# Kernel tuning notes

Measured on AMD Instinct MI355X. Metric: run time of the kernel, lower is better.

## Reference

```python
import jax, jax.numpy as jnp
import numpy as np

N = 25000      # nodes per type
E = 300000     # weight-edge rows
K = 16         # neighbors
F = 64         # in_feat
A = 64         # atten_dim
DW = 64        # weight_dim
CB = 8         # num_bit_conv
CV = 8         # num_vector_conv
OUT = 64       # out_feat
IN_K = CB * F + CV * (3 + 2 + 1)


def setup_inputs() -> dict:
    key = jax.random.key(0)
    ks = jax.random.split(key, 40)
    s = 0.05
    d = {}
    d['eu'] = jax.random.normal(ks[0], (N, F), jnp.float32)
    d['ei'] = jax.random.normal(ks[1], (N, F), jnp.float32)
    d['et'] = jax.random.normal(ks[2], (N, F), jnp.float32)
    d['ew'] = jax.random.normal(ks[3], (E, DW), jnp.float32)
    names = ['u_iw_j', 'u_tw_j', 'i_uw_j', 'i_tw_j', 't_uw_j', 't_iw_j']
    for i, nm in enumerate(names):
        d[nm] = jax.random.randint(ks[4 + i], (N, K), 0, N, jnp.int64 if jax.config.jax_enable_x64 else jnp.int32)
        d[nm.replace('_j', '_w')] = jax.random.randint(ks[10 + i], (N, K), 0, E, jnp.int64 if jax.config.jax_enable_x64 else jnp.int32)
    # per-type Attention1 params: user, item, tag
    for i, t in enumerate(['user', 'item', 'tag']):
        b = 16 + 4 * i
        d[f'W1_{t}'] = jax.random.normal(ks[b], (F + DW, A), jnp.float32) * s
        d[f'W2_{t}'] = jax.random.normal(ks[b + 1], (F, A), jnp.float32) * s
        d[f'b_{t}'] = jax.random.normal(ks[b + 2], (1, A), jnp.float32) * s
        d[f'v_{t}'] = jax.random.normal(ks[b + 3], (1, A), jnp.float32) * s
    d['U'] = jax.random.normal(ks[28], (F, A), jnp.float32) * s
    d['q'] = jax.random.normal(ks[29], (1, A), jnp.float32) * s
    d['p'] = jax.random.normal(ks[30], (1, A), jnp.float32) * s
    d['W_bit'] = jax.random.normal(ks[31], (CB, 3), jnp.float32) * s       # Conv2d(1,CB,(3,1))
    d['W_vec1'] = jax.random.normal(ks[32], (CV, 1, F), jnp.float32) * s   # Conv2d(1,CV,(1,F))
    d['W_vec2'] = jax.random.normal(ks[33], (CV, 2, F), jnp.float32) * s
    d['W_vec3'] = jax.random.normal(ks[34], (CV, 3, F), jnp.float32) * s
    d['Wf'] = jax.random.normal(ks[35], (IN_K, OUT), jnp.float32) * s
    d['bf'] = jax.random.normal(ks[36], (1, OUT), jnp.float32) * s
    return d


def _atten1(ev, ej, ew, v_j, v_w, W1, W2, b, v):
    ejp = jnp.concatenate([jnp.zeros((1, ej.shape[1]), ej.dtype), ej], axis=0)
    ewp = jnp.concatenate([jnp.zeros((1, ew.shape[1]), ew.dtype), ew], axis=0)
    eNj = ejp[v_j]                                  # [N,K,F]
    eNw = ewp[v_w]                                  # [N,K,DW]
    eNv = jnp.broadcast_to(ev[:, None, :], (ev.shape[0], v_j.shape[1], ev.shape[1]))
    eN_vw = jnp.concatenate([eNv, eNw], axis=-1)    # [N,K,F+DW]
    av = jnp.einsum('nkd,da->nka', eN_vw, W1) + jnp.einsum('nkf,fa->nka', eNj, W2) + b
    x = jax.nn.relu(av) @ v.T                       # [N,K,1]
    a = jax.nn.softmax(x, axis=1)
    return jnp.sum(a * eNj, axis=1)                 # [N,F]


def _atten2(u, i, t, U, q, p):
    uit = jnp.stack([u, i, t], axis=1)              # [N,3,F]
    x = jnp.einsum('nsf,fa->nsa', uit, U) + q
    x = jax.nn.relu(x) @ p.T                        # [N,3,1]
    b = jax.nn.softmax(x, axis=1)
    return b * uit                                  # [N,3,F]


def _conv(eN, W_bit, W_vec1, W_vec2, W_vec3):
    # eN: [N,3,F]
    bit = jax.nn.relu(jnp.einsum('njf,cj->ncf', eN, W_bit))       # [N,CB,F]
    bit = bit.reshape(bit.shape[0], -1)
    vec = []
    for j, W in ((1, W_vec1), (2, W_vec2), (3, W_vec3)):
        win = jnp.stack([eN[:, s:s + j, :] for s in range(3 - j + 1)], axis=1)  # [N,4-j,j,F]
        y = jax.nn.relu(jnp.einsum('nsjf,cjf->ncs', win, W))       # [N,CV,4-j]
        vec.append(y.reshape(y.shape[0], -1))
    return jnp.concatenate([bit] + vec, axis=1)                    # [N,IN_K]


def _forward(eu, ei, et, ew, params, idx):
    (W1u, W2u, bu, vu, W1i, W2i, bi, vi, W1t, W2t, bt, vt,
     U, q, p, W_bit, W_vec1, W_vec2, W_vec3, Wf, bf) = params
    (u_iw_j, u_iw_w, u_tw_j, u_tw_w, i_uw_j, i_uw_w,
     i_tw_j, i_tw_w, t_uw_j, t_uw_w, t_iw_j, t_iw_w) = idx
    eu_iN = _atten1(eu, ei, ew, u_iw_j, u_iw_w, W1i, W2i, bi, vi)
    eu_tN = _atten1(eu, et, ew, u_tw_j, u_tw_w, W1t, W2t, bt, vt)
    ei_uN = _atten1(ei, eu, ew, i_uw_j, i_uw_w, W1u, W2u, bu, vu)
    ei_tN = _atten1(ei, et, ew, i_tw_j, i_tw_w, W1t, W2t, bt, vt)
    et_uN = _atten1(et, eu, ew, t_uw_j, t_uw_w, W1u, W2u, bu, vu)
    et_iN = _atten1(et, ei, ew, t_iw_j, t_iw_w, W1i, W2i, bi, vi)
    euN = _atten2(eu, eu_iN, eu_tN, U, q, p)
    eiN = _atten2(ei_uN, ei, ei_tN, U, q, p)
    etN = _atten2(et_uN, et_iN, et, U, q, p)
    out = []
    for eN in (euN, eiN, etN):
        c = _conv(eN, W_bit, W_vec1, W_vec2, W_vec3)
        out.append(jax.nn.relu(c @ Wf + bf))
    return tuple(out)


def reference(eu, ei, et, ew,
              u_iw_j, u_iw_w, u_tw_j, u_tw_w, i_uw_j, i_uw_w, i_tw_j, i_tw_w,
              t_uw_j, t_uw_w, t_iw_j, t_iw_w,
              W1_user, W2_user, b_user, v_user,
              W1_item, W2_item, b_item, v_item,
              W1_tag, W2_tag, b_tag, v_tag,
              U, q, p, W_bit, W_vec1, W_vec2, W_vec3, Wf, bf):
    params = (W1_user, W2_user, b_user, v_user, W1_item, W2_item, b_item, v_item,
              W1_tag, W2_tag, b_tag, v_tag, U, q, p, W_bit, W_vec1, W_vec2, W_vec3, Wf, bf)
    idx = (u_iw_j, u_iw_w, u_tw_j, u_tw_w, i_uw_j, i_uw_w,
           i_tw_j, i_tw_w, t_uw_j, t_uw_w, t_iw_j, t_iw_w)
    return _forward(eu, ei, et, ew, params, idx)
```

## Files before the change

kernel.cpp:

```cpp
#include <hip/hip_runtime.h>
#include <math.h>

#define NN 25000
#define EE 300000
#define NT 1563
#define NT64 391
#define ET64 4688

typedef __attribute__((ext_vector_type(8))) short bf16x8;
typedef __attribute__((ext_vector_type(4))) float f32x4;
typedef __attribute__((ext_vector_type(2))) float f32x2;

__device__ __forceinline__ unsigned short f2bf(float f) {
    union { float f; unsigned u; } a; a.f = f;
    unsigned r = (a.u + 0x7fffu + ((a.u >> 16) & 1u)) >> 16;
    return (unsigned short)r;
}
__device__ __forceinline__ unsigned pack2(float lo, float hi) {
    return (unsigned)f2bf(lo) | ((unsigned)f2bf(hi) << 16);
}
__device__ __forceinline__ float bflo(unsigned p) {
    union { unsigned u; float f; } a; a.u = p << 16; return a.f;
}
__device__ __forceinline__ float bfhi(unsigned p) {
    union { unsigned u; float f; } a; a.u = p & 0xffff0000u; return a.f;
}
__device__ __forceinline__ unsigned packfp8x4(float a, float b, float c, float d) {
    int v = __builtin_amdgcn_cvt_pk_fp8_f32(a, b, 0, 0);
    v = __builtin_amdgcn_cvt_pk_fp8_f32(c, d, v, 1);
    return (unsigned)v;
}

__global__ __launch_bounds__(256) void head_kernel(
    const float* __restrict__ ew,
    const float* __restrict__ eu, const float* __restrict__ ei, const float* __restrict__ et,
    const float* __restrict__ W1u, const float* __restrict__ W1i, const float* __restrict__ W1t,
    const float* __restrict__ W2u, const float* __restrict__ W2i, const float* __restrict__ W2t,
    const float* __restrict__ bu, const float* __restrict__ bi, const float* __restrict__ bt,
    unsigned char* __restrict__ gw8, unsigned* __restrict__ preB,
    unsigned char* __restrict__ JG)
{
    __shared__ __align__(16) unsigned short stA[64 * 72];
    __shared__ __align__(16) float cS[64 * 68];
    const int t = threadIdx.x;
    const int lane = t & 63, wv = t >> 6;
    const int l15 = lane & 15, quad = lane >> 4;
    const int cw = wv * 16 + l15;
    const int bx = blockIdx.x;

    if (bx < ET64) {
        if (bx == 0 && t < 48) {
            int w = t >> 4;
            ((unsigned*)(gw8 + (size_t)w * (EE + 1) * 64))[t & 15] = 0u;
        }
        const float* Ws[3] = { W1u + 4096, W1i + 4096, W1t + 4096 };
        bf16x8 bf[3][2];
        #pragma unroll
        for (int w = 0; w < 3; ++w)
            #pragma unroll
            for (int ks = 0; ks < 2; ++ks)
                #pragma unroll
                for (int j = 0; j < 8; ++j)
                    bf[w][ks][j] = (short)f2bf(Ws[w][(ks * 32 + quad * 8 + j) * 64 + cw]);

        const int rowBase = bx * 64;
        #pragma unroll
        for (int i = 0; i < 4; ++i) {
            int idx = t + i * 256;
            int row = idx >> 4, cg = idx & 15;
            int gr = rowBase + row;
            float4 v4 = (gr < EE) ? *(const float4*)(ew + (size_t)gr * 64 + cg * 4)
                                  : make_float4(0.f, 0.f, 0.f, 0.f);
            uint2 pk = { pack2(v4.x, v4.y), pack2(v4.z, v4.w) };
            *(uint2*)&stA[row * 72 + cg * 4] = pk;
        }
        __syncthreads();
        bf16x8 af[4][2];
        #pragma unroll
        for (int m = 0; m < 4; ++m)
            #pragma unroll
            for (int ks = 0; ks < 2; ++ks)
                af[m][ks] = *(const bf16x8*)&stA[(m * 16 + l15) * 72 + ks * 32 + quad * 8];

        #pragma unroll
        for (int w = 0; w < 3; ++w) {
            if (w) __syncthreads();
            f32x4 acc[4];
            #pragma unroll
            for (int m = 0; m < 4; ++m) {
                acc[m].x = 0; acc[m].y = 0; acc[m].z = 0; acc[m].w = 0;
                #pragma unroll
                for (int ks = 0; ks < 2; ++ks)
                    acc[m] = __builtin_amdgcn_mfma_f32_16x16x32_bf16(af[m][ks], bf[w][ks], acc[m], 0, 0, 0);
                #pragma unroll
                for (int r = 0; r < 4; ++r)
                    cS[(m * 16 + quad * 4 + r) * 68 + cw] = acc[m][r];
            }
            __syncthreads();
            unsigned char* outg = gw8 + (size_t)w * (EE + 1) * 64 + 64;
            #pragma unroll
            for (int i = 0; i < 2; ++i) {
                int task = t + i * 256;
                int row = task >> 3, seg = task & 7;
                int gr = rowBase + row;
                if (gr < EE) {
                    float4 a = *(const float4*)&cS[row * 68 + seg * 8];
                    float4 b = *(const float4*)&cS[row * 68 + seg * 8 + 4];
                    uint2 pk = { packfp8x4(a.x, a.y, a.z, a.w),
                                 packfp8x4(b.x, b.y, b.z, b.w) };
                    *(uint2*)(outg + (size_t)gr * 64 + seg * 8) = pk;
                }
            }
        }
    } else {
        const int yy = bx - ET64;
        const int y = yy / NT64;
        const int rowBase = (yy - y * NT64) * 64;
        if (rowBase == 0 && t < 48)
            ((unsigned*)(JG + (size_t)y * (NN + 1) * 192))[t] = 0u;
        const float* X; const float* Wa; const float* Wb; const float* W2;
        const float* ba; const float* bb; int oa, ob;
        switch (y) {
            case 0:  X = eu; Wa = W1i; ba = bi; oa = 0; Wb = W1t; bb = bt; ob = 1; W2 = W2u; break;
            case 1:  X = ei; Wa = W1u; ba = bu; oa = 2; Wb = W1t; bb = bt; ob = 3; W2 = W2i; break;
            default: X = et; Wa = W1u; ba = bu; oa = 4; Wb = W1i; bb = bi; ob = 5; W2 = W2t; break;
        }
        const float* Ws[3] = { Wa, Wb, W2 };
        const float bias_cw[3] = { ba[cw], bb[cw], 0.f };
        bf16x8 bf[3][2];
        #pragma unroll
        for (int w = 0; w < 3; ++w)
            #pragma unroll
            for (int ks = 0; ks < 2; ++ks)
                #pragma unroll
                for (int j = 0; j < 8; ++j)
                    bf[w][ks][j] = (short)f2bf(Ws[w][(ks * 32 + quad * 8 + j) * 64 + cw]);

        #pragma unroll
        for (int i = 0; i < 4; ++i) {
            int idx = t + i * 256;
            int row = idx >> 4, cg = idx & 15;
            int gr = rowBase + row;
            float4 v4 = (gr < NN) ? *(const float4*)(X + (size_t)gr * 64 + cg * 4)
                                  : make_float4(0.f, 0.f, 0.f, 0.f);
            uint2 pk = { pack2(v4.x, v4.y), pack2(v4.z, v4.w) };
            *(uint2*)&stA[row * 72 + cg * 4] = pk;
        }
        __syncthreads();
        bf16x8 af[4][2];
        #pragma unroll
        for (int m = 0; m < 4; ++m)
            #pragma unroll
            for (int ks = 0; ks < 2; ++ks)
                af[m][ks] = *(const bf16x8*)&stA[(m * 16 + l15) * 72 + ks * 32 + quad * 8];

        #pragma unroll
        for (int w = 0; w < 3; ++w) {
            if (w) __syncthreads();
            f32x4 acc[4];
            #pragma unroll
            for (int m = 0; m < 4; ++m) {
                acc[m].x = 0; acc[m].y = 0; acc[m].z = 0; acc[m].w = 0;
                #pragma unroll
                for (int ks = 0; ks < 2; ++ks)
                    acc[m] = __builtin_amdgcn_mfma_f32_16x16x32_bf16(af[m][ks], bf[w][ks], acc[m], 0, 0, 0);
                #pragma unroll
                for (int r = 0; r < 4; ++r)
                    cS[(m * 16 + quad * 4 + r) * 68 + cw] = acc[m][r] + bias_cw[w];
            }
            __syncthreads();
            #pragma unroll
            for (int i = 0; i < 2; ++i) {
                int task = t + i * 256;
                int row = task >> 3, seg = task & 7;
                int gr = rowBase + row;
                if (gr >= NN) continue;
                float4 a = *(const float4*)&cS[row * 68 + seg * 8];
                float4 b = *(const float4*)&cS[row * 68 + seg * 8 + 4];
                if (w < 2) {
                    int oi = (w == 0) ? oa : ob;
                    uint4 pk = { pack2(a.x, a.y), pack2(a.z, a.w),
                                 pack2(b.x, b.y), pack2(b.z, b.w) };
                    *(uint4*)(preB + ((size_t)oi * NN + gr) * 32 + seg * 4) = pk;
                } else {
                    unsigned char* dst = JG + ((size_t)y * (NN + 1) + gr + 1) * 192;
                    uint2 gj = { packfp8x4(a.x, a.y, a.z, a.w),
                                 packfp8x4(b.x, b.y, b.z, b.w) };
                    *(uint2*)(dst + seg * 8) = gj;
                    uint4 ej = *(const uint4*)&stA[row * 72 + seg * 8];
                    *(uint4*)(dst + 64 + seg * 16) = ej;
                }
            }
        }
    }
}

__global__ __launch_bounds__(256) void atten1_kernel(
    const unsigned* __restrict__ preB, const unsigned char* __restrict__ gw8,
    const unsigned char* __restrict__ JG,
    const float* __restrict__ vu, const float* __restrict__ vi, const float* __restrict__ vt,
    const int* __restrict__ u_iw_j, const int* __restrict__ u_iw_w,
    const int* __restrict__ u_tw_j, const int* __restrict__ u_tw_w,
    const int* __restrict__ i_uw_j, const int* __restrict__ i_uw_w,
    const int* __restrict__ i_tw_j, const int* __restrict__ i_tw_w,
    const int* __restrict__ t_uw_j, const int* __restrict__ t_uw_w,
    const int* __restrict__ t_iw_j, const int* __restrict__ t_iw_w,
    unsigned* __restrict__ aoB)
{
    const int y = blockIdx.y;
    const int* Vj; const int* Vw; const float* v; int g;
    switch (y) {
        case 0:  Vj = u_iw_j; Vw = u_iw_w; v = vi; g = 1; break;
        case 1:  Vj = u_tw_j; Vw = u_tw_w; v = vt; g = 2; break;
        case 2:  Vj = i_uw_j; Vw = i_uw_w; v = vu; g = 0; break;
        case 3:  Vj = i_tw_j; Vw = i_tw_w; v = vt; g = 2; break;
        case 4:  Vj = t_uw_j; Vw = t_uw_w; v = vu; g = 0; break;
        default: Vj = t_iw_j; Vw = t_iw_w; v = vi; g = 1; break;
    }
    const unsigned* pre = preB + (size_t)y * NN * 32;
    const unsigned char* gw = gw8 + (size_t)g * (EE + 1) * 64;
    const unsigned char* jg = JG + (size_t)g * (NN + 1) * 192;
    unsigned*            out = aoB + (size_t)y * NN * 32;

    const int lane = threadIdx.x & 63;
    const int n = blockIdx.x * 4 + (threadIdx.x >> 6);
    const int q = lane >> 4, r = lane & 15;

    const uint2 prep = *(const uint2*)(pre + (size_t)n * 32 + 2 * r);
    const float pf0 = bflo(prep.x), pf1 = bfhi(prep.x);
    const float pf2 = bflo(prep.y), pf3 = bfhi(prep.y);
    const float4 v4 = *(const float4*)(v + r * 4);

    const int4 wi = *(const int4*)(Vw + n * 16 + q * 4);
    const int4 ji = *(const int4*)(Vj + n * 16 + q * 4);
    const int wid[4] = { wi.x, wi.y, wi.z, wi.w };
    const int jid[4] = { ji.x, ji.y, ji.z, ji.w };

    unsigned gwv[4], gjv[4]; uint2 ejv[4];
    #pragma unroll
    for (int i = 0; i < 4; ++i)
        gwv[i] = *(const unsigned*)(gw + (size_t)wid[i] * 64 + r * 4);
    #pragma unroll
    for (int i = 0; i < 4; ++i) {
        const unsigned char* row = jg + (size_t)jid[i] * 192;
        gjv[i] = *(const unsigned*)(row + r * 4);
        ejv[i] = *(const uint2*)(row + 64 + r * 8);
    }

    float xk[4];
    #pragma unroll
    for (int i = 0; i < 4; ++i) {
        f32x2 g01 = __builtin_amdgcn_cvt_pk_f32_fp8((int)gwv[i], false);
        f32x2 g23 = __builtin_amdgcn_cvt_pk_f32_fp8((int)gwv[i], true);
        f32x2 j01 = __builtin_amdgcn_cvt_pk_f32_fp8((int)gjv[i], false);
        f32x2 j23 = __builtin_amdgcn_cvt_pk_f32_fp8((int)gjv[i], true);
        float x =          fmaxf(pf0 + g01.x + j01.x, 0.f) * v4.x;
        x = fmaf(fmaxf(pf1 + g01.y + j01.y, 0.f), v4.y, x);
        x = fmaf(fmaxf(pf2 + g23.x + j23.x, 0.f), v4.z, x);
        x = fmaf(fmaxf(pf3 + g23.y + j23.y, 0.f), v4.w, x);
        x += __shfl_xor(x, 1, 64);
        x += __shfl_xor(x, 2, 64);
        x += __shfl_xor(x, 4, 64);
        x += __shfl_xor(x, 8, 64);
        xk[i] = x;
    }
    float m = fmaxf(fmaxf(xk[0], xk[1]), fmaxf(xk[2], xk[3]));
    m = fmaxf(m, __shfl_xor(m, 16, 64));
    m = fmaxf(m, __shfl_xor(m, 32, 64));
    float e0 = __expf(xk[0] - m), e1 = __expf(xk[1] - m);
    float e2 = __expf(xk[2] - m), e3 = __expf(xk[3] - m);
    float s = (e0 + e1) + (e2 + e3);
    s += __shfl_xor(s, 16, 64);
    s += __shfl_xor(s, 32, 64);
    const float inv = 1.f / s;

    float a0 = 0.f, a1 = 0.f, a2 = 0.f, a3 = 0.f;
    const float wgt[4] = { e0 * inv, e1 * inv, e2 * inv, e3 * inv };
    #pragma unroll
    for (int i = 0; i < 4; ++i) {
        a0 = fmaf(wgt[i], bflo(ejv[i].x), a0);
        a1 = fmaf(wgt[i], bfhi(ejv[i].x), a1);
        a2 = fmaf(wgt[i], bflo(ejv[i].y), a2);
        a3 = fmaf(wgt[i], bfhi(ejv[i].y), a3);
    }
    a0 += __shfl_xor(a0, 16, 64); a0 += __shfl_xor(a0, 32, 64);
    a1 += __shfl_xor(a1, 16, 64); a1 += __shfl_xor(a1, 32, 64);
    a2 += __shfl_xor(a2, 16, 64); a2 += __shfl_xor(a2, 32, 64);
    a3 += __shfl_xor(a3, 16, 64); a3 += __shfl_xor(a3, 32, 64);
    if (q == 0) {
        uint2 pk = { pack2(a0, a1), pack2(a2, a3) };
        *(uint2*)(out + (size_t)n * 32 + 2 * r) = pk;
    }
}

__global__ __launch_bounds__(256, 3) void tail_kernel(
    const float* __restrict__ eu, const float* __restrict__ ei, const float* __restrict__ et,
    const unsigned* __restrict__ aoB,
    const float* __restrict__ U, const float* __restrict__ q, const float* __restrict__ p,
    const float* __restrict__ Wbit, const float* __restrict__ Wv1,
    const float* __restrict__ Wv2, const float* __restrict__ Wv3,
    const float* __restrict__ Wf, const float* __restrict__ bfv,
    float* __restrict__ out)
{
    __shared__ __align__(16) unsigned short uitA[48 * 72];
    __shared__ __align__(16) unsigned short eNA[48 * 72];
    __shared__ __align__(16) unsigned short wcf[6 * 64 * 8];
    __shared__ __align__(16) unsigned short c_sh[16 * 584];
    __shared__ float G_sh[48 * 52];
    __shared__ float xpart[4 * 48];
    __shared__ float bcoef[16 * 4];

    const int t = threadIdx.x;
    const int lane = t & 63;
    const int wv = t >> 6;
    const int l15 = lane & 15;
    const int quad = lane >> 4;
    const int type = blockIdx.y;
    const float* xf = (type == 0) ? eu : (type == 1) ? ei : et;
    const int cw = wv * 16 + l15;
    const float qv = q[cw], pv = p[cw], bfb = bfv[cw];

    float wb[8][3];
    #pragma unroll
    for (int c = 0; c < 8; ++c)
        #pragma unroll
        for (int s = 0; s < 3; ++s) wb[c][s] = Wbit[c * 3 + s];

    bf16x8 ufrag[2];
    #pragma unroll
    for (int ks = 0; ks < 2; ++ks)
        #pragma unroll
        for (int j = 0; j < 8; ++j) {
            int f = ks * 32 + quad * 8 + j;
            ufrag[ks][j] = (short)f2bf(U[f * 64 + cw]);
        }
    bf16x8 wff[18];
    #pragma unroll
    for (int ks = 0; ks < 18; ++ks)
        #pragma unroll
        for (int j = 0; j < 8; ++j) {
            int k = ks * 32 + quad * 8 + j;
            float w = (k < 560) ? Wf[(size_t)k * 64 + cw] : 0.f;
            wff[ks][j] = (short)f2bf(w);
        }
    for (int slot = t; slot < 384; slot += 256) {
        int fi = slot >> 6, l = slot & 63;
        int nt_ = fi >> 1, ks = fi & 1;
        int r = nt_ * 16 + (l & 15);
        unsigned short vals[8];
        #pragma unroll
        for (int j = 0; j < 8; ++j) {
            int f = ks * 32 + (l >> 4) * 8 + j;
            float wv_;
            if (r < 8)       wv_ = Wv1[r * 64 + f];
            else if (r < 24) { int u = r - 8;  wv_ = Wv2[(u >> 1) * 128 + (u & 1) * 64 + f]; }
            else             { int u = r - 24; wv_ = Wv3[(u / 3) * 192 + (u % 3) * 64 + f]; }
            vals[j] = f2bf(wv_);
        }
        uint4 pk = { (unsigned)vals[0] | ((unsigned)vals[1] << 16),
                     (unsigned)vals[2] | ((unsigned)vals[3] << 16),
                     (unsigned)vals[4] | ((unsigned)vals[5] << 16),
                     (unsigned)vals[6] | ((unsigned)vals[7] << 16) };
        *(uint4*)&wcf[slot * 8] = pk;
    }

    for (int tile = blockIdx.x; tile < NT; tile += gridDim.x) {
        const int nodeBase = tile * 16;
        __syncthreads();
        #pragma unroll
        for (int i = 0; i < 3; ++i) {
            int idx = t + i * 256;
            int row = idx >> 4, cg = idx & 15;
            int nl = row / 3, s = row - nl * 3;
            int n = nodeBase + nl;
            uint2 pk;
            if (s == type) {
                float4 v4 = (n < NN) ? *(const float4*)(xf + (size_t)n * 64 + cg * 4)
                                     : make_float4(0.f, 0.f, 0.f, 0.f);
                pk.x = pack2(v4.x, v4.y); pk.y = pack2(v4.z, v4.w);
            } else {
                int aoidx = (type == 0) ? (s - 1)
                          : (type == 1) ? ((s == 0) ? 2 : 3)
                                        : ((s == 0) ? 4 : 5);
                pk = (n < NN) ? *(const uint2*)(aoB + ((size_t)aoidx * NN + n) * 32 + cg * 2)
                              : make_uint2(0u, 0u);
            }
            *(uint2*)&uitA[row * 72 + cg * 4] = pk;
        }
        __syncthreads();
        {
            f32x4 av[3];
            #pragma unroll
            for (int mt = 0; mt < 3; ++mt) { av[mt].x = 0; av[mt].y = 0; av[mt].z = 0; av[mt].w = 0; }
            #pragma unroll
            for (int mt = 0; mt < 3; ++mt)
                #pragma unroll
                for (int ks = 0; ks < 2; ++ks) {
                    bf16x8 a = *(const bf16x8*)&uitA[(mt * 16 + l15) * 72 + ks * 32 + quad * 8];
                    av[mt] = __builtin_amdgcn_mfma_f32_16x16x32_bf16(a, ufrag[ks], av[mt], 0, 0, 0);
                }
            #pragma unroll
            for (int mt = 0; mt < 3; ++mt)
                #pragma unroll
                for (int r = 0; r < 4; ++r) {
                    float val = fmaxf(av[mt][r] + qv, 0.f) * pv;
                    val += __shfl_xor(val, 1, 64); val += __shfl_xor(val, 2, 64);
                    val += __shfl_xor(val, 4, 64); val += __shfl_xor(val, 8, 64);
                    if (l15 == 0) xpart[wv * 48 + mt * 16 + quad * 4 + r] = val;
                }
        }
        __syncthreads();
        if (t < 16) {
            float xv[3];
            #pragma unroll
            for (int s = 0; s < 3; ++s)
                xv[s] = xpart[t * 3 + s] + xpart[48 + t * 3 + s]
                      + xpart[96 + t * 3 + s] + xpart[144 + t * 3 + s];
            float mm = fmaxf(xv[0], fmaxf(xv[1], xv[2]));
            float e0 = __expf(xv[0] - mm), e1 = __expf(xv[1] - mm), e2 = __expf(xv[2] - mm);
            float inv = 1.f / (e0 + e1 + e2);
            bcoef[t * 4 + 0] = e0 * inv; bcoef[t * 4 + 1] = e1 * inv; bcoef[t * 4 + 2] = e2 * inv;
        }
        __syncthreads();
        #pragma unroll
        for (int i = 0; i < 2; ++i) {
            int task = t + i * 256;
            int nl = task >> 5, fp = task & 31;
            float b0 = bcoef[nl * 4], b1 = bcoef[nl * 4 + 1], b2 = bcoef[nl * 4 + 2];
            unsigned u0 = *(const unsigned*)&uitA[(nl * 3 + 0) * 72 + fp * 2];
            unsigned u1 = *(const unsigned*)&uitA[(nl * 3 + 1) * 72 + fp * 2];
            unsigned u2 = *(const unsigned*)&uitA[(nl * 3 + 2) * 72 + fp * 2];
            float e0l = b0 * bflo(u0), e0h = b0 * bfhi(u0);
            float e1l = b1 * bflo(u1), e1h = b1 * bfhi(u1);
            float e2l = b2 * bflo(u2), e2h = b2 * bfhi(u2);
            *(unsigned*)&eNA[(nl * 3 + 0) * 72 + fp * 2] = pack2(e0l, e0h);
            *(unsigned*)&eNA[(nl * 3 + 1) * 72 + fp * 2] = pack2(e1l, e1h);
            *(unsigned*)&eNA[(nl * 3 + 2) * 72 + fp * 2] = pack2(e2l, e2h);
            #pragma unroll
            for (int c = 0; c < 8; ++c) {
                float lo = fmaxf(wb[c][0] * e0l + wb[c][1] * e1l + wb[c][2] * e2l, 0.f);
                float hi = fmaxf(wb[c][0] * e0h + wb[c][1] * e1h + wb[c][2] * e2h, 0.f);
                *(unsigned*)&c_sh[nl * 584 + c * 64 + fp * 2] = pack2(lo, hi);
            }
        }
        __syncthreads();
        #pragma unroll
        for (int pi = 0; pi < 3; ++pi) {
            int pr = wv + pi * 4;
            if (pr < 9) {
                int mm = pr / 3, nn_ = pr - mm * 3;
                f32x4 g; g.x = 0; g.y = 0; g.z = 0; g.w = 0;
                #pragma unroll
                for (int ks = 0; ks < 2; ++ks) {
                    bf16x8 a = *(const bf16x8*)&eNA[(mm * 16 + l15) * 72 + ks * 32 + quad * 8];
                    bf16x8 b = *(const bf16x8*)&wcf[((nn_ * 2 + ks) * 64 + lane) * 8];
                    g = __builtin_amdgcn_mfma_f32_16x16x32_bf16(a, b, g, 0, 0, 0);
                }
                #pragma unroll
                for (int r = 0; r < 4; ++r)
                    G_sh[(mm * 16 + quad * 4 + r) * 52 + nn_ * 16 + l15] = g[r];
            }
        }
        __syncthreads();
        #pragma unroll
        for (int i = 0; i < 4; ++i) {
            int task = t + i * 256;
            int vvv = task >> 4, nl = task & 15;
            unsigned short res = 0;
            if (vvv < 24) {
                int c = vvv / 3, s = vvv - c * 3;
                res = f2bf(fmaxf(G_sh[(nl * 3 + s) * 52 + c], 0.f));
            } else if (vvv < 40) {
                int u = vvv - 24, c = u >> 1, s = u & 1;
                float val = G_sh[(nl * 3 + s) * 52 + 8 + 2 * c]
                          + G_sh[(nl * 3 + s + 1) * 52 + 8 + 2 * c + 1];
                res = f2bf(fmaxf(val, 0.f));
            } else if (vvv < 48) {
                int c = vvv - 40;
                float val = G_sh[(nl * 3 + 0) * 52 + 24 + 3 * c]
                          + G_sh[(nl * 3 + 1) * 52 + 24 + 3 * c + 1]
                          + G_sh[(nl * 3 + 2) * 52 + 24 + 3 * c + 2];
                res = f2bf(fmaxf(val, 0.f));
            }
            c_sh[nl * 584 + 512 + vvv] = res;
        }
        __syncthreads();
        {
            f32x4 acc; acc.x = 0; acc.y = 0; acc.z = 0; acc.w = 0;
            const unsigned short* ap = &c_sh[l15 * 584 + quad * 8];
            #pragma unroll
            for (int ks = 0; ks < 18; ++ks) {
                bf16x8 a = *(const bf16x8*)(ap + ks * 32);
                acc = __builtin_amdgcn_mfma_f32_16x16x32_bf16(a, wff[ks], acc, 0, 0, 0);
            }
            float* outT = out + (size_t)type * NN * 64;
            #pragma unroll
            for (int r = 0; r < 4; ++r) {
                int node = nodeBase + quad * 4 + r;
                if (node < NN) outT[(size_t)node * 64 + cw] = fmaxf(acc[r] + bfb, 0.f);
            }
        }
    }
}

extern "C" void kernel_launch(void* const* d_in, const int* in_sizes, int n_in,
                              void* d_out, int out_size, void* d_ws, size_t ws_size,
                              hipStream_t stream)
{
    const float* eu = (const float*)d_in[0];
    const float* ei = (const float*)d_in[1];
    const float* et = (const float*)d_in[2];
    const float* ew = (const float*)d_in[3];
    const int* u_iw_j = (const int*)d_in[4];
    const int* u_iw_w = (const int*)d_in[5];
    const int* u_tw_j = (const int*)d_in[6];
    const int* u_tw_w = (const int*)d_in[7];
    const int* i_uw_j = (const int*)d_in[8];
    const int* i_uw_w = (const int*)d_in[9];
    const int* i_tw_j = (const int*)d_in[10];
    const int* i_tw_w = (const int*)d_in[11];
    const int* t_uw_j = (const int*)d_in[12];
    const int* t_uw_w = (const int*)d_in[13];
    const int* t_iw_j = (const int*)d_in[14];
    const int* t_iw_w = (const int*)d_in[15];
    const float* W1_user = (const float*)d_in[16];
    const float* W2_user = (const float*)d_in[17];
    const float* b_user  = (const float*)d_in[18];
    const float* v_user  = (const float*)d_in[19];
    const float* W1_item = (const float*)d_in[20];
    const float* W2_item = (const float*)d_in[21];
    const float* b_item  = (const float*)d_in[22];
    const float* v_item  = (const float*)d_in[23];
    const float* W1_tag  = (const float*)d_in[24];
    const float* W2_tag  = (const float*)d_in[25];
    const float* b_tag   = (const float*)d_in[26];
    const float* v_tag   = (const float*)d_in[27];
    const float* U    = (const float*)d_in[28];
    const float* q    = (const float*)d_in[29];
    const float* p    = (const float*)d_in[30];
    const float* Wbit = (const float*)d_in[31];
    const float* Wv1  = (const float*)d_in[32];
    const float* Wv2  = (const float*)d_in[33];
    const float* Wv3  = (const float*)d_in[34];
    const float* Wf   = (const float*)d_in[35];
    const float* bfv  = (const float*)d_in[36];
    float* out = (float*)d_out;

    unsigned char* gw8 = (unsigned char*)d_ws;
    unsigned* preB = (unsigned*)(gw8 + (size_t)3 * (EE + 1) * 64);
    unsigned char* JG = (unsigned char*)(preB + (size_t)6 * NN * 32);
    unsigned* aoB = (unsigned*)(JG + (size_t)3 * (NN + 1) * 192);

    const dim3 blk(256);

    head_kernel<<<ET64 + 3 * NT64, blk, 0, stream>>>(
        ew, eu, ei, et,
        W1_user, W1_item, W1_tag, W2_user, W2_item, W2_tag,
        b_user, b_item, b_tag, gw8, preB, JG);

    atten1_kernel<<<dim3(NN / 4, 6), blk, 0, stream>>>(
        preB, gw8, JG, v_user, v_item, v_tag,
        u_iw_j, u_iw_w, u_tw_j, u_tw_w, i_uw_j, i_uw_w,
        i_tw_j, i_tw_w, t_uw_j, t_uw_w, t_iw_j, t_iw_w, aoB);

    tail_kernel<<<dim3(256, 3), blk, 0, stream>>>(
        eu, ei, et, aoB,
        U, q, p, Wbit, Wv1, Wv2, Wv3, Wf, bfv, out);
}
```

Measured before the change: 399.1 us.

## Map two nodes per wavefront in atten1 and drop tail softmax barrier stage

Result: no change. 405.0 us (+1.5%).

```diff
diff --git a/kernel.cpp b/kernel.cpp
--- a/kernel.cpp
+++ b/kernel.cpp
@@ -223,73 +223,99 @@
     unsigned*            out = aoB + (size_t)y * NN * 32;
 
     const int lane = threadIdx.x & 63;
-    const int n = blockIdx.x * 4 + (threadIdx.x >> 6);
-    const int q = lane >> 4, r = lane & 15;
-
-    const uint2 prep = *(const uint2*)(pre + (size_t)n * 32 + 2 * r);
-    const float pf0 = bflo(prep.x), pf1 = bfhi(prep.x);
-    const float pf2 = bflo(prep.y), pf3 = bfhi(prep.y);
-    const float4 v4 = *(const float4*)(v + r * 4);
+    const int wv = threadIdx.x >> 6;
+    const int h = lane >> 5, l = lane & 31;
+    const int q = l >> 3, r = l & 7;
+    const int n = blockIdx.x * 8 + wv * 2 + h;
+
+    const uint4 prep = *(const uint4*)(pre + (size_t)n * 32 + r * 4);
+    f32x2 pf2[4];
+    pf2[0].x = bflo(prep.x); pf2[0].y = bfhi(prep.x);
+    pf2[1].x = bflo(prep.y); pf2[1].y = bfhi(prep.y);
+    pf2[2].x = bflo(prep.z); pf2[2].y = bfhi(prep.z);
+    pf2[3].x = bflo(prep.w); pf2[3].y = bfhi(prep.w);
+    const float4 va = *(const float4*)(v + r * 8);
+    const float4 vb = *(const float4*)(v + r * 8 + 4);
+    f32x2 v2[4];
+    v2[0].x = va.x; v2[0].y = va.y;  v2[1].x = va.z; v2[1].y = va.w;
+    v2[2].x = vb.x; v2[2].y = vb.y;  v2[3].x = vb.z; v2[3].y = vb.w;
 
     const int4 wi = *(const int4*)(Vw + n * 16 + q * 4);
     const int4 ji = *(const int4*)(Vj + n * 16 + q * 4);
     const int wid[4] = { wi.x, wi.y, wi.z, wi.w };
     const int jid[4] = { ji.x, ji.y, ji.z, ji.w };
 
-    unsigned gwv[4], gjv[4]; uint2 ejv[4];
+    uint2 gwv[4], gjv[4]; uint4 ejv[4];
     #pragma unroll
     for (int i = 0; i < 4; ++i)
-        gwv[i] = *(const unsigned*)(gw + (size_t)wid[i] * 64 + r * 4);
+        gwv[i] = *(const uint2*)(gw + (size_t)wid[i] * 64 + r * 8);
     #pragma unroll
     for (int i = 0; i < 4; ++i) {
         const unsigned char* row = jg + (size_t)jid[i] * 192;
-        gjv[i] = *(const unsigned*)(row + r * 4);
-        ejv[i] = *(const uint2*)(row + 64 + r * 8);
+        gjv[i] = *(const uint2*)(row + r * 8);
+        ejv[i] = *(const uint4*)(row + 64 + r * 16);
     }
 
     float xk[4];
     #pragma unroll
     for (int i = 0; i < 4; ++i) {
-        f32x2 g01 = __builtin_amdgcn_cvt_pk_f32_fp8((int)gwv[i], false);
-        f32x2 g23 = __builtin_amdgcn_cvt_pk_f32_fp8((int)gwv[i], true);
-        f32x2 j01 = __builtin_amdgcn_cvt_pk_f32_fp8((int)gjv[i], false);
-        f32x2 j23 = __builtin_amdgcn_cvt_pk_f32_fp8((int)gjv[i], true);
-        float x =          fmaxf(pf0 + g01.x + j01.x, 0.f) * v4.x;
-        x = fmaf(fmaxf(pf1 + g01.y + j01.y, 0.f), v4.y, x);
-        x = fmaf(fmaxf(pf2 + g23.x + j23.x, 0.f), v4.z, x);
-        x = fmaf(fmaxf(pf3 + g23.y + j23.y, 0.f), v4.w, x);
+        f32x2 acc2; acc2.x = 0.f; acc2.y = 0.f;
+        #pragma unroll
+        for (int w = 0; w < 2; ++w) {
+            unsigned gword = (w == 0) ? gwv[i].x : gwv[i].y;
+            unsigned jword = (w == 0) ? gjv[i].x : gjv[i].y;
+            f32x2 glo = __builtin_amdgcn_cvt_pk_f32_fp8((int)gword, false);
+            f32x2 ghi = __builtin_amdgcn_cvt_pk_f32_fp8((int)gword, true);
+            f32x2 jlo = __builtin_amdgcn_cvt_pk_f32_fp8((int)jword, false);
+            f32x2 jhi = __builtin_amdgcn_cvt_pk_f32_fp8((int)jword, true);
+            f32x2 t0 = pf2[w * 2] + glo + jlo;
+            f32x2 t1 = pf2[w * 2 + 1] + ghi + jhi;
+            t0.x = fmaxf(t0.x, 0.f); t0.y = fmaxf(t0.y, 0.f);
+            t1.x = fmaxf(t1.x, 0.f); t1.y = fmaxf(t1.y, 0.f);
+            acc2 += t0 * v2[w * 2];
+            acc2 += t1 * v2[w * 2 + 1];
+        }
+        float x = acc2.x + acc2.y;
         x += __shfl_xor(x, 1, 64);
         x += __shfl_xor(x, 2, 64);
         x += __shfl_xor(x, 4, 64);
-        x += __shfl_xor(x, 8, 64);
         xk[i] = x;
     }
     float m = fmaxf(fmaxf(xk[0], xk[1]), fmaxf(xk[2], xk[3]));
+    m = fmaxf(m, __shfl_xor(m, 8, 64));
     m = fmaxf(m, __shfl_xor(m, 16, 64));
-    m = fmaxf(m, __shfl_xor(m, 32, 64));
     float e0 = __expf(xk[0] - m), e1 = __expf(xk[1] - m);
     float e2 = __expf(xk[2] - m), e3 = __expf(xk[3] - m);
     float s = (e0 + e1) + (e2 + e3);
+    s += __shfl_xor(s, 8, 64);
     s += __shfl_xor(s, 16, 64);
-    s += __shfl_xor(s, 32, 64);
     const float inv = 1.f / s;
-
-    float a0 = 0.f, a1 = 0.f, a2 = 0.f, a3 = 0.f;
     const float wgt[4] = { e0 * inv, e1 * inv, e2 * inv, e3 * inv };
+
+    f32x2 ac[4];
+    #pragma unroll
+    for (int j = 0; j < 4; ++j) { ac[j].x = 0.f; ac[j].y = 0.f; }
     #pragma unroll
     for (int i = 0; i < 4; ++i) {
-        a0 = fmaf(wgt[i], bflo(ejv[i].x), a0);
-        a1 = fmaf(wgt[i], bfhi(ejv[i].x), a1);
-        a2 = fmaf(wgt[i], bflo(ejv[i].y), a2);
-        a3 = fmaf(wgt[i], bfhi(ejv[i].y), a3);
-    }
-    a0 += __shfl_xor(a0, 16, 64); a0 += __shfl_xor(a0, 32, 64);
-    a1 += __shfl_xor(a1, 16, 64); a1 += __shfl_xor(a1, 32, 64);
-    a2 += __shfl_xor(a2, 16, 64); a2 += __shfl_xor(a2, 32, 64);
-    a3 += __shfl_xor(a3, 16, 64); a3 += __shfl_xor(a3, 32, 64);
+        const float wg = wgt[i];
+        f32x2 e01; e01.x = bflo(ejv[i].x); e01.y = bfhi(ejv[i].x);
+        f32x2 e23; e23.x = bflo(ejv[i].y); e23.y = bfhi(ejv[i].y);
+        f32x2 e45; e45.x = bflo(ejv[i].z); e45.y = bfhi(ejv[i].z);
+        f32x2 e67; e67.x = bflo(ejv[i].w); e67.y = bfhi(ejv[i].w);
+        ac[0] += e01 * wg; ac[1] += e23 * wg;
+        ac[2] += e45 * wg; ac[3] += e67 * wg;
+    }
+    float a[8] = { ac[0].x, ac[0].y, ac[1].x, ac[1].y,
+                   ac[2].x, ac[2].y, ac[3].x, ac[3].y };
+    #pragma unroll
+    for (int j = 0; j < 8; ++j) {
+        a[j] += __shfl_xor(a[j], 8, 64);
+        a[j] += __shfl_xor(a[j], 16, 64);
+    }
     if (q == 0) {
-        uint2 pk = { pack2(a0, a1), pack2(a2, a3) };
-        *(uint2*)(out + (size_t)n * 32 + 2 * r) = pk;
+        uint4 pk = { pack2(a[0], a[1]), pack2(a[2], a[3]),
+                     pack2(a[4], a[5]), pack2(a[6], a[7]) };
+        *(uint4*)(out + (size_t)n * 32 + r * 4) = pk;
     }
 }
 
@@ -308,7 +334,6 @@
     __shared__ __align__(16) unsigned short c_sh[16 * 584];
     __shared__ float G_sh[48 * 52];
     __shared__ float xpart[4 * 48];
-    __shared__ float bcoef[16 * 4];
 
     const int t = threadIdx.x;
     const int lane = t & 63;
@@ -366,7 +391,6 @@
 
     for (int tile = blockIdx.x; tile < NT; tile += gridDim.x) {
         const int nodeBase = tile * 16;
-        __syncthreads();
         #pragma unroll
         for (int i = 0; i < 3; ++i) {
             int idx = t + i * 256;
@@ -410,23 +434,20 @@
                 }
         }
         __syncthreads();
-        if (t < 16) {
-            float xv[3];
-            #pragma unroll
-            for (int s = 0; s < 3; ++s)
-                xv[s] = xpart[t * 3 + s] + xpart[48 + t * 3 + s]
-                      + xpart[96 + t * 3 + s] + xpart[144 + t * 3 + s];
-            float mm = fmaxf(xv[0], fmaxf(xv[1], xv[2]));
-            float e0 = __expf(xv[0] - mm), e1 = __expf(xv[1] - mm), e2 = __expf(xv[2] - mm);
-            float inv = 1.f / (e0 + e1 + e2);
-            bcoef[t * 4 + 0] = e0 * inv; bcoef[t * 4 + 1] = e1 * inv; bcoef[t * 4 + 2] = e2 * inv;
-        }
-        __syncthreads();
         #pragma unroll
         for (int i = 0; i < 2; ++i) {
             int task = t + i * 256;
             int nl = task >> 5, fp = task & 31;
-            float b0 = bcoef[nl * 4], b1 = bcoef[nl * 4 + 1], b2 = bcoef[nl * 4 + 2];
+            float xv0 = xpart[nl * 3 + 0] + xpart[48 + nl * 3 + 0]
+                      + xpart[96 + nl * 3 + 0] + xpart[144 + nl * 3 + 0];
+            float xv1 = xpart[nl * 3 + 1] + xpart[48 + nl * 3 + 1]
+                      + xpart[96 + nl * 3 + 1] + xpart[144 + nl * 3 + 1];
+            float xv2 = xpart[nl * 3 + 2] + xpart[48 + nl * 3 + 2]
+                      + xpart[96 + nl * 3 + 2] + xpart[144 + nl * 3 + 2];
+            float mm = fmaxf(xv0, fmaxf(xv1, xv2));
+            float ex0 = __expf(xv0 - mm), ex1 = __expf(xv1 - mm), ex2 = __expf(xv2 - mm);
+            float inv = 1.f / (ex0 + ex1 + ex2);
+            float b0 = ex0 * inv, b1 = ex1 * inv, b2 = ex2 * inv;
             unsigned u0 = *(const unsigned*)&uitA[(nl * 3 + 0) * 72 + fp * 2];
             unsigned u1 = *(const unsigned*)&uitA[(nl * 3 + 1) * 72 + fp * 2];
             unsigned u2 = *(const unsigned*)&uitA[(nl * 3 + 2) * 72 + fp * 2];
@@ -558,7 +579,7 @@
         W1_user, W1_item, W1_tag, W2_user, W2_item, W2_tag,
         b_user, b_item, b_tag, gw8, preB, JG);
 
-    atten1_kernel<<<dim3(NN / 4, 6), blk, 0, stream>>>(
+    atten1_kernel<<<dim3(NN / 8, 6), blk, 0, stream>>>(
         preB, gw8, JG, v_user, v_item, v_tag,
         u_iw_j, u_iw_w, u_tw_j, u_tw_w, i_uw_j, i_uw_w,
         i_tw_j, i_tw_w, t_uw_j, t_uw_w, t_iw_j, t_iw_w, aoB);
```
